# Performance work log

Measured on AMD Instinct MI355X. Metric: run time of the kernel, lower is better.

Reference implementation:

```python
import jax, jax.numpy as jnp
import numpy as np

WIN = 8     # sliding-chunk window size (Long2DSCSelfAttention default w=8)
HEADS = 8   # num_heads


def setup_inputs() -> dict:
    key = jax.random.key(0)
    ks = jax.random.split(key, 3)
    B, C, H, W = 4, 512, 64, 64
    x = jax.random.normal(ks[0], (B, C, H, W), jnp.float32)
    w_qkv = jax.random.normal(ks[1], (3 * C, C), jnp.float32) * 0.02
    b_qkv = jnp.zeros((3 * C,), jnp.float32)
    w_proj = jax.random.normal(ks[2], (C, C), jnp.float32) * 0.02
    b_proj = jnp.zeros((C,), jnp.float32)
    return {"x": x, "w_qkv": w_qkv, "b_qkv": b_qkv, "w_proj": w_proj, "b_proj": b_proj}


def _chunk(t, nh, nw, win):
    B, _, _, h, d = t.shape
    t = t.reshape(B, nh, win, nw, win, h, d)
    return t.transpose(0, 5, 1, 3, 2, 4, 6).reshape(B, h, nh, nw, win * win, d)


def reference(x, w_qkv, b_qkv, w_proj, b_proj):
    B, C, H, W = x.shape
    win, heads = WIN, HEADS
    d = C // heads
    nh, nw = H // win, W // win
    m = win * win  # tokens per chunk

    xf = x.transpose(0, 2, 3, 1)                      # [B,H,W,C]
    qkv = xf @ w_qkv.T + b_qkv                        # [B,H,W,3C]
    qkv = qkv.reshape(B, H, W, 3, heads, d)
    q = _chunk(qkv[..., 0, :, :], nh, nw, win)        # [B,h,nh,nw,m,d]
    k = _chunk(qkv[..., 1, :, :], nh, nw, win)
    v = _chunk(qkv[..., 2, :, :], nh, nw, win)

    # pad chunk grid by one chunk on each side; gather 3x3 chunk neighborhoods
    kp = jnp.pad(k, ((0, 0), (0, 0), (1, 1), (1, 1), (0, 0), (0, 0)))
    vp = jnp.pad(v, ((0, 0), (0, 0), (1, 1), (1, 1), (0, 0), (0, 0)))
    k9 = jnp.concatenate([kp[:, :, i:i + nh, j:j + nw] for i in range(3) for j in range(3)], axis=4)  # [B,h,nh,nw,9m,d]
    v9 = jnp.concatenate([vp[:, :, i:i + nh, j:j + nw] for i in range(3) for j in range(3)], axis=4)

    # validity mask for neighbor chunks at the image boundary
    valid = jnp.pad(jnp.ones((nh, nw), bool), ((1, 1), (1, 1)))
    vmask = jnp.concatenate(
        [jnp.repeat(valid[i:i + nh, j:j + nw][..., None], m, axis=-1) for i in range(3) for j in range(3)],
        axis=-1)                                      # [nh,nw,9m]

    scale = float(d) ** -0.5
    attn = jnp.einsum('bhxyqd,bhxykd->bhxyqk', q * scale, k9)      # [B,h,nh,nw,m,9m]
    neg = jnp.asarray(-1e9, attn.dtype)
    attn = jnp.where(vmask[None, None, :, :, None, :], attn, neg)
    attn = jax.nn.softmax(attn, axis=-1)
    out = jnp.einsum('bhxyqk,bhxykd->bhxyqd', attn, v9)            # [B,h,nh,nw,m,d]

    out = out.reshape(B, heads, nh, nw, win, win, d)
    out = out.transpose(0, 2, 4, 3, 5, 1, 6).reshape(B, H, W, C)
    out = out @ w_proj.T + b_proj
    return out.transpose(0, 3, 1, 2)                               # [B,C,H,W]
```

## Files before the change

kernel.cpp:

```cpp
#include <hip/hip_runtime.h>
#include <cstdint>
#include <cstddef>

namespace {

constexpr int kC = 512;
constexpr int kHW = 4096;
constexpr int kHeads = 8;
constexpr int kChunkElems = 64 * 64;

typedef float f32x4 __attribute__((ext_vector_type(4)));
typedef _Float16 f16x8 __attribute__((ext_vector_type(8)));
union FragU { uint4 u; f16x8 h; };

__device__ __forceinline__ ushort f16rn(float x) {
  _Float16 h = (_Float16)x;
  ushort u;
  __builtin_memcpy(&u, &h, 2);
  return u;
}
__device__ __forceinline__ uint pack2(ushort a, ushort b) {
  return (uint)a | ((uint)b << 16);
}
__device__ __forceinline__ float fexp2(float x) {
  return exp2f(x);
}
__device__ __forceinline__ uint pkrtz(float a, float b) {
  auto h = __builtin_amdgcn_cvt_pkrtz(a, b);
  uint u;
  __builtin_memcpy(&u, &h, 4);
  return u;
}
__device__ __forceinline__ void gld16(const void* g, void* lds) {
  __builtin_amdgcn_global_load_lds(
      (const __attribute__((address_space(1))) uint32_t*)g,
      (__attribute__((address_space(3))) uint32_t*)lds, 16, 0, 0);
}

__global__ __launch_bounds__(256)
void convw16_kernel(const float* __restrict__ w, ushort* __restrict__ wh)
{
  int idx = (blockIdx.x * 256 + threadIdx.x) * 8;
  float4 v0 = *(const float4*)(w + idx);
  float4 v1 = *(const float4*)(w + idx + 4);
  float xs[8] = {v0.x, v0.y, v0.z, v0.w, v1.x, v1.y, v1.z, v1.w};
  ushort hh[8];
#pragma unroll
  for (int e = 0; e < 8; ++e) hh[e] = f16rn(xs[e]);
  *(uint4*)(wh + idx) = make_uint4(pack2(hh[0], hh[1]), pack2(hh[2], hh[3]),
                                   pack2(hh[4], hh[5]), pack2(hh[6], hh[7]));
}

__global__ __launch_bounds__(256)
void convx_kernel(const float* __restrict__ x, ushort* __restrict__ xt)
{
  __shared__ float LT[64][68];
  const int tid = threadIdx.x;
  const int t0 = blockIdx.x * 64;
  const int c0 = blockIdx.y * 64;
  const int b  = blockIdx.z;
  const float* xb = x + (size_t)b * kC * kHW;

#pragma unroll
  for (int u = 0; u < 4; ++u) {
    int idx = tid + u * 256;
    int rc = idx >> 4;
    int t4 = (idx & 15) << 2;
    float4 val = *(const float4*)(xb + (size_t)(c0 + rc) * kHW + t0 + t4);
    LT[t4 + 0][rc] = val.x;
    LT[t4 + 1][rc] = val.y;
    LT[t4 + 2][rc] = val.z;
    LT[t4 + 3][rc] = val.w;
  }
  __syncthreads();
#pragma unroll
  for (int u = 0; u < 4; ++u) {
    int idx = tid + u * 256;
    int rt = idx >> 4;
    int c4 = (idx & 15) << 2;
    float4 v = *(const float4*)&LT[rt][c4];
    size_t o = ((size_t)b * kHW + t0 + rt) * kC + c0 + c4;
    *(ushort4*)(xt + o) = make_ushort4(f16rn(v.x), f16rn(v.y),
                                       f16rn(v.z), f16rn(v.w));
  }
}

__global__ __launch_bounds__(256)
void qkv_mfma_kernel(const ushort* __restrict__ xt,
                     const ushort* __restrict__ wq,
                     const float* __restrict__ bqkv,
                     ushort* __restrict__ qo, ushort* __restrict__ ko,
                     ushort* __restrict__ vo)
{
  __shared__ __align__(16) ushort As[2][128 * 64];
  __shared__ __align__(16) ushort Bs[2][128 * 64];

  const int tid  = threadIdx.x;
  const int lane = tid & 63;
  const int wv   = tid >> 6;
  const int quad = lane >> 4;
  const int l15  = lane & 15;
  const int wm = wv & 1, wn = wv >> 1;
  const int m0 = blockIdx.x * 128;
  const int n0 = blockIdx.y * 128;
  const int b  = blockIdx.z;

  const ushort* xb = xt + (size_t)b * kHW * kC;

  auto stage = [&](int buf, int k0) {
#pragma unroll
    for (int ii = 0; ii < 4; ++ii) {
      int i = wv * 4 + ii;
      int m = i * 8 + (lane >> 3);
      int gch = (lane & 7) ^ (m & 7);
      size_t goA = (size_t)(m0 + m) * kC + k0 + gch * 8;
      gld16(xb + goA, (char*)&As[buf][0] + i * 1024);
      size_t goB = (size_t)(n0 + m) * kC + k0 + gch * 8;
      gld16(wq + goB, (char*)&Bs[buf][0] + i * 1024);
    }
  };

  f32x4 acc[4][4];
#pragma unroll
  for (int i = 0; i < 4; ++i)
#pragma unroll
    for (int j = 0; j < 4; ++j) acc[i][j] = (f32x4){0.f, 0.f, 0.f, 0.f};

  stage(0, 0);
  asm volatile("s_waitcnt vmcnt(0)" ::: "memory");
  asm volatile("s_barrier" ::: "memory");

  for (int kt = 0; kt < 8; ++kt) {
    const int cur = kt & 1;
    if (kt < 7) stage(cur ^ 1, (kt + 1) * 64);

    const ushort* Ac = &As[cur][0];
    const ushort* Bc = &Bs[cur][0];
#pragma unroll
    for (int s = 0; s < 2; ++s) {
      const int gq = s * 4 + quad;
      FragU aA[4], bB[4];
#pragma unroll
      for (int mi = 0; mi < 4; ++mi) {
        int mr = wm * 64 + mi * 16 + l15;
        int off = mr * 64 + ((gq ^ (mr & 7)) * 8);
        aA[mi].u = *(const uint4*)&Ac[off];
      }
#pragma unroll
      for (int ni = 0; ni < 4; ++ni) {
        int nr = wn * 64 + ni * 16 + l15;
        int off = nr * 64 + ((gq ^ (nr & 7)) * 8);
        bB[ni].u = *(const uint4*)&Bc[off];
      }
#pragma unroll
      for (int mi = 0; mi < 4; ++mi)
#pragma unroll
        for (int ni = 0; ni < 4; ++ni)
          acc[mi][ni] = __builtin_amdgcn_mfma_f32_16x16x32_f16(aA[mi].h, bB[ni].h, acc[mi][ni], 0, 0, 0);
    }

    asm volatile("s_waitcnt lgkmcnt(0)" ::: "memory");
    if (kt < 7) asm volatile("s_waitcnt vmcnt(0)" ::: "memory");
    asm volatile("s_barrier" ::: "memory");
  }

  const int sec = n0 >> 9;
  const int jwbase = n0 + wn * 64;
  const int head = (jwbase >> 6) & 7;
  const size_t hbb = ((size_t)b * kHeads + head) * 64;
  float biasv[4];
#pragma unroll
  for (int ni = 0; ni < 4; ++ni) biasv[ni] = bqkv[jwbase + ni * 16 + l15];

  if (sec == 2) {
#pragma unroll
    for (int ni = 0; ni < 4; ++ni) {
      int dd = ni * 16 + l15;
#pragma unroll
      for (int mi = 0; mi < 4; ++mi) {
        int t0t = m0 + wm * 64 + mi * 16 + quad * 4;
        int h = t0t >> 6, w = t0t & 63;
        int cy = h >> 3, iy = h & 7, cx = w >> 3, ix = w & 7;
        size_t cb = (hbb + cy * 8 + cx) * (size_t)kChunkElems;
        int tokb = iy * 8 + ix;
        ushort hh[4];
#pragma unroll
        for (int r = 0; r < 4; ++r) hh[r] = f16rn(acc[mi][ni][r] + biasv[ni]);
        *(ushort4*)(vo + cb + (size_t)dd * 64 + tokb) = make_ushort4(hh[0], hh[1], hh[2], hh[3]);
      }
    }
  } else {
    ushort* dst = (sec == 0) ? qo : ko;
    const float sc = (sec == 0) ? 0.125f * 1.44269504089f : 1.0f;
    ushort* tH = &As[0][0] + wv * 1152;
    const int ltok = lane >> 2;
    const int dd0 = (lane & 3) * 16;
#pragma unroll
    for (int mi = 0; mi < 4; ++mi) {
#pragma unroll
      for (int ni = 0; ni < 4; ++ni)
#pragma unroll
        for (int r = 0; r < 4; ++r)
          tH[(quad * 4 + r) * 68 + ni * 16 + l15] =
              f16rn((acc[mi][ni][r] + biasv[ni]) * sc);
      int tg = m0 + wm * 64 + mi * 16 + ltok;
      int h = tg >> 6, w = tg & 63;
      int cy = h >> 3, iy = h & 7, cx = w >> 3, ix = w & 7;
      size_t cb = (hbb + cy * 8 + cx) * (size_t)kChunkElems
                + (size_t)(iy * 8 + ix) * 64 + dd0;
      uint4 h0 = *(const uint4*)&tH[ltok * 68 + dd0];
      uint4 h1 = *(const uint4*)&tH[ltok * 68 + dd0 + 8];
      *(uint4*)(dst + cb) = h0;
      *(uint4*)(dst + cb + 8) = h1;
    }
  }
}

__global__ __launch_bounds__(256)
void attn_mfma_kernel(const ushort* __restrict__ qg, const ushort* __restrict__ kg,
                      const ushort* __restrict__ vg,
                      ushort* __restrict__ ao)
{
  __shared__ __align__(16) ushort KB[4096], VB[4096];
  __shared__ __align__(16) ushort Ps[4 * 16 * 72];

  const int tid  = threadIdx.x;
  const int lane = tid & 63;
  const int wv   = tid >> 6;
  const int quad = lane >> 4;
  const int l15  = lane & 15;

  const int bx = blockIdx.x;
  const int g  = (bx & 7) * 4 + ((bx >> 3) >> 6);
  const int c  = (bx >> 3) & 63;
  const int b = g >> 3, head = g & 7;
  const int cy = c >> 3, cx = c & 7;

  const size_t hb = (size_t)b * kHeads + head;
  const size_t gbase = hb * 64 * (size_t)kChunkElems;
  const size_t cbase = gbase + (size_t)c * (size_t)kChunkElems;

  FragU aQ0, aQ1;
  {
    const ushort* qr = qg + cbase + (size_t)(wv * 16 + l15) * 64 + quad * 8;
    aQ0.u = *(const uint4*)(qr);
    aQ1.u = *(const uint4*)(qr + 32);
  }

  const int boff = ((lane >> 3) * 64) + (((lane & 7) ^ (lane >> 3)) * 8);
  const ushort* kgB = kg + gbase + boff + (size_t)(wv * 2) * 512;
  const ushort* vgB = vg + gbase + boff + (size_t)(wv * 2) * 512;
  char* kDst0 = (char*)KB + (wv * 2) * 1024;
  char* vDst0 = (char*)VB + (wv * 2) * 1024;

  int kvOff0[4], kvOff1[4];
  {
    const int sw = l15 & 7;
#pragma unroll
    for (int nt = 0; nt < 4; ++nt) {
      int row = nt * 16 + l15;
      kvOff0[nt] = row * 64 + ((quad ^ sw) * 8);
      kvOff1[nt] = row * 64 + (((4 + quad) ^ sw) * 8);
    }
  }

  ushort* PsW = Ps + wv * 1152;
  ushort* pWr = PsW + l15 * 72 + quad * 4;
  const ushort* pRd = PsW + l15 * 72 + quad * 8;

  unsigned long long list = 0ull;
  int cnt = 0;
#pragma unroll
  for (int p = 0; p < 9; ++p) {
    const int dy = p / 3 - 1, dx = p % 3 - 1;
    int ny = cy + dy, nx = cx + dx;
    if ((unsigned)ny < 8u && (unsigned)nx < 8u) {
      list |= (unsigned long long)(ny * 8 + nx) << (6 * cnt);
      ++cnt;
    }
  }

  f32x4 o[4];
#pragma unroll
  for (int r = 0; r < 4; ++r) o[r] = (f32x4){0.f, 0.f, 0.f, 0.f};
  float rsum = 0.f;

  {
    int ch0 = (int)(list & 63);
    const ushort* pk = kgB + (size_t)ch0 * kChunkElems;
    gld16(pk, kDst0);
    gld16(pk + 512, kDst0 + 1024);
    const ushort* pv = vgB + (size_t)ch0 * kChunkElems;
    gld16(pv, vDst0);
    gld16(pv + 512, vDst0 + 1024);
  }

  for (int i = 0; i < cnt; ++i) {
    const bool more = (i + 1 < cnt);
    const int chn = (int)((list >> (6 * (i + 1))) & 63);

    asm volatile("s_waitcnt vmcnt(2)" ::: "memory");
    asm volatile("s_barrier" ::: "memory");

    FragU kf[8];
#pragma unroll
    for (int nt = 0; nt < 4; ++nt) {
      kf[nt * 2].u     = *(const uint4*)&KB[kvOff0[nt]];
      kf[nt * 2 + 1].u = *(const uint4*)&KB[kvOff1[nt]];
    }
    asm volatile("s_waitcnt lgkmcnt(0)" ::: "memory");
    asm volatile("s_waitcnt vmcnt(0)" ::: "memory");
    asm volatile("s_barrier" ::: "memory");

    if (more) {
      const ushort* pk = kgB + (size_t)chn * kChunkElems;
      gld16(pk, kDst0);
      gld16(pk + 512, kDst0 + 1024);
    }

    f32x4 s[4];
#pragma unroll
    for (int nt = 0; nt < 4; ++nt) s[nt] = (f32x4){0.f, 0.f, 0.f, 0.f};
#pragma unroll
    for (int nt = 0; nt < 4; ++nt) {
      s[nt] = __builtin_amdgcn_mfma_f32_16x16x32_f16(kf[nt * 2].h, aQ0.h, s[nt], 0, 0, 0);
      s[nt] = __builtin_amdgcn_mfma_f32_16x16x32_f16(kf[nt * 2 + 1].h, aQ1.h, s[nt], 0, 0, 0);
    }

#pragma unroll
    for (int nt = 0; nt < 4; ++nt) {
      float e0 = fexp2(s[nt][0]);
      float e1 = fexp2(s[nt][1]);
      float e2 = fexp2(s[nt][2]);
      float e3 = fexp2(s[nt][3]);
      rsum += (e0 + e1) + (e2 + e3);
      *(uint2*)(pWr + nt * 16) = make_uint2(pkrtz(e0, e1), pkrtz(e2, e3));
    }

    FragU aP0, aP1;
    aP0.u = *(const uint4*)(pRd);
    aP1.u = *(const uint4*)(pRd + 32);

#pragma unroll
    for (int nt = 0; nt < 4; ++nt) {
      FragU v0, v1;
      v0.u = *(const uint4*)&VB[kvOff0[nt]];
      v1.u = *(const uint4*)&VB[kvOff1[nt]];
      o[nt] = __builtin_amdgcn_mfma_f32_16x16x32_f16(v0.h, aP0.h, o[nt], 0, 0, 0);
      o[nt] = __builtin_amdgcn_mfma_f32_16x16x32_f16(v1.h, aP1.h, o[nt], 0, 0, 0);
    }

    asm volatile("s_waitcnt lgkmcnt(0)" ::: "memory");
    asm volatile("s_barrier" ::: "memory");
    if (more) {
      const ushort* pv = vgB + (size_t)chn * kChunkElems;
      gld16(pv, vDst0);
      gld16(pv + 512, vDst0 + 1024);
    }
  }

  rsum += __shfl_xor(rsum, 16, 64);
  rsum += __shfl_xor(rsum, 32, 64);
  const float inv = 1.0f / rsum;

  const int trg = wv * 16 + l15;
  const int hp = cy * 8 + (trg >> 3);
  const int wp = cx * 8 + (trg & 7);
  const size_t obase = ((size_t)b * kHW + hp * 64 + wp) * (size_t)kC + head * 64;

#pragma unroll
  for (int nt = 0; nt < 4; ++nt) {
    float v0 = o[nt][0] * inv;
    float v1 = o[nt][1] * inv;
    float v2 = o[nt][2] * inv;
    float v3 = o[nt][3] * inv;
    *(ushort4*)(ao + obase + nt * 16 + quad * 4) =
        make_ushort4(f16rn(v0), f16rn(v1), f16rn(v2), f16rn(v3));
  }
}

__global__ __launch_bounds__(256)
void proj_mfma_kernel(const ushort* __restrict__ ao,
                      const ushort* __restrict__ wp,
                      const float* __restrict__ bproj,
                      float* __restrict__ out)
{
  __shared__ __align__(16) ushort As[2][128 * 64];
  __shared__ __align__(16) ushort Bs[2][64 * 64];

  const int tid  = threadIdx.x;
  const int lane = tid & 63;
  const int wv   = tid >> 6;
  const int quad = lane >> 4;
  const int l15  = lane & 15;
  const int wm = wv & 1, wn = wv >> 1;
  const int n0g = blockIdx.x * 64;
  const int m0  = blockIdx.y * 128;
  const int b   = n0g >> 12;
  const int tl0 = n0g & 4095;

  auto stage = [&](int buf, int k0) {
#pragma unroll
    for (int ii = 0; ii < 4; ++ii) {
      int i = wv * 4 + ii;
      int m = i * 8 + (lane >> 3);
      int gch = (lane & 7) ^ (m & 7);
      size_t goA = (size_t)(m0 + m) * kC + k0 + gch * 8;
      gld16(wp + goA, (char*)&As[buf][0] + i * 1024);
    }
#pragma unroll
    for (int ii = 0; ii < 2; ++ii) {
      int i = wv * 2 + ii;
      int m = i * 8 + (lane >> 3);
      int gch = (lane & 7) ^ (m & 7);
      size_t goB = (size_t)(n0g + m) * kC + k0 + gch * 8;
      gld16(ao + goB, (char*)&Bs[buf][0] + i * 1024);
    }
  };

  f32x4 acc[4][2];
#pragma unroll
  for (int i = 0; i < 4; ++i)
#pragma unroll
    for (int j = 0; j < 2; ++j) acc[i][j] = (f32x4){0.f, 0.f, 0.f, 0.f};

  stage(0, 0);
  asm volatile("s_waitcnt vmcnt(0)" ::: "memory");
  asm volatile("s_barrier" ::: "memory");

  for (int kt = 0; kt < 8; ++kt) {
    const int cur = kt & 1;
    if (kt < 7) stage(cur ^ 1, (kt + 1) * 64);

    const ushort* Ac = &As[cur][0];
    const ushort* Bc = &Bs[cur][0];
#pragma unroll
    for (int s = 0; s < 2; ++s) {
      const int gq = s * 4 + quad;
      FragU aA[4], bB[2];
#pragma unroll
      for (int mi = 0; mi < 4; ++mi) {
        int mr = wm * 64 + mi * 16 + l15;
        int off = mr * 64 + ((gq ^ (mr & 7)) * 8);
        aA[mi].u = *(const uint4*)&Ac[off];
      }
#pragma unroll
      for (int ni = 0; ni < 2; ++ni) {
        int nr = wn * 32 + ni * 16 + l15;
        int off = nr * 64 + ((gq ^ (nr & 7)) * 8);
        bB[ni].u = *(const uint4*)&Bc[off];
      }
#pragma unroll
      for (int mi = 0; mi < 4; ++mi)
#pragma unroll
        for (int ni = 0; ni < 2; ++ni)
          acc[mi][ni] = __builtin_amdgcn_mfma_f32_16x16x32_f16(aA[mi].h, bB[ni].h, acc[mi][ni], 0, 0, 0);
    }

    asm volatile("s_waitcnt lgkmcnt(0)" ::: "memory");
    if (kt < 7) asm volatile("s_waitcnt vmcnt(0)" ::: "memory");
    asm volatile("s_barrier" ::: "memory");
  }

#pragma unroll
  for (int mi = 0; mi < 4; ++mi)
#pragma unroll
    for (int r = 0; r < 4; ++r) {
      int c = m0 + wm * 64 + mi * 16 + quad * 4 + r;
      float bias = bproj[c];
      size_t rowb = ((size_t)b * kC + c) * (size_t)kHW + tl0 + wn * 32;
#pragma unroll
      for (int ni = 0; ni < 2; ++ni)
        out[rowb + ni * 16 + l15] = acc[mi][ni][r] + bias;
    }
}

}

extern "C" void kernel_launch(void* const* d_in, const int* in_sizes, int n_in,
                              void* d_out, int out_size, void* d_ws, size_t ws_size,
                              hipStream_t stream)
{
  const float* x     = (const float*)d_in[0];
  const float* wqkv  = (const float*)d_in[1];
  const float* bqkv  = (const float*)d_in[2];
  const float* wproj = (const float*)d_in[3];
  const float* bproj = (const float*)d_in[4];
  float* out = (float*)d_out;

  const size_t seg = (size_t)2048 * kChunkElems;
  ushort* base = (ushort*)d_ws;
  ushort* qb = base + 0 * seg;
  ushort* kb = base + 1 * seg;
  ushort* vb = base + 2 * seg;
  ushort* xt = base + 3 * seg;
  ushort* ao = xt;
  ushort* wqh = base + 5 * seg;
  ushort* wp16 = qb;

  convw16_kernel<<<dim3(384), 256, 0, stream>>>(wqkv, wqh);
  convx_kernel<<<dim3(64, 8, 4), 256, 0, stream>>>(x, xt);
  qkv_mfma_kernel<<<dim3(32, 12, 4), 256, 0, stream>>>(xt, wqh, bqkv,
                                                       qb, kb, vb);
  attn_mfma_kernel<<<dim3(2048), 256, 0, stream>>>(qb, kb, vb, ao);
  convw16_kernel<<<dim3(128), 256, 0, stream>>>(wproj, wp16);
  proj_mfma_kernel<<<dim3(256, 4), 256, 0, stream>>>(ao, wp16, bproj, out);
}
```

Before: 192.3 us.

## Enlarge QKV GEMM tile to 256x128 with 512 threads and swizzled block order

The QKV projection GEMM now runs 512-thread blocks computing 256x128 output tiles, so each staged weight tile is reused across twice as many rows. A flattened block-index swizzle reorders tiles to improve L2 locality. All LDS fragments for both k-substeps are loaded up front, and the MFMA section runs under raised wave priority. The larger tile raises LDS use and per-block register pressure, which may lower occupancy. The epilogue must still map the 4x2 wave layout correctly.

```diff
diff --git a/kernel.cpp b/kernel.cpp
--- a/kernel.cpp
+++ b/kernel.cpp
@@ -85,14 +85,14 @@
   }
 }
 
-__global__ __launch_bounds__(256)
+__global__ __launch_bounds__(512)
 void qkv_mfma_kernel(const ushort* __restrict__ xt,
                      const ushort* __restrict__ wq,
                      const float* __restrict__ bqkv,
                      ushort* __restrict__ qo, ushort* __restrict__ ko,
                      ushort* __restrict__ vo)
 {
-  __shared__ __align__(16) ushort As[2][128 * 64];
+  __shared__ __align__(16) ushort As[2][256 * 64];
   __shared__ __align__(16) ushort Bs[2][128 * 64];
 
   const int tid  = threadIdx.x;
@@ -100,10 +100,15 @@
   const int wv   = tid >> 6;
   const int quad = lane >> 4;
   const int l15  = lane & 15;
-  const int wm = wv & 1, wn = wv >> 1;
-  const int m0 = blockIdx.x * 128;
-  const int n0 = blockIdx.y * 128;
-  const int b  = blockIdx.z;
+  const int wm = wv & 3;
+  const int wn = wv >> 2;
+
+  const int flat = blockIdx.x + 16 * (blockIdx.y + 12 * blockIdx.z);
+  const int swz  = (flat & 7) * 96 + (flat >> 3);
+  const int m0 = (swz & 15) * 256;
+  const int t2 = swz >> 4;
+  const int n0 = (t2 % 12) * 128;
+  const int b  = t2 / 12;
 
   const ushort* xb = xt + (size_t)b * kHW * kC;
 
@@ -113,10 +118,16 @@
       int i = wv * 4 + ii;
       int m = i * 8 + (lane >> 3);
       int gch = (lane & 7) ^ (m & 7);
-      size_t goA = (size_t)(m0 + m) * kC + k0 + gch * 8;
-      gld16(xb + goA, (char*)&As[buf][0] + i * 1024);
-      size_t goB = (size_t)(n0 + m) * kC + k0 + gch * 8;
-      gld16(wq + goB, (char*)&Bs[buf][0] + i * 1024);
+      gld16(xb + (size_t)(m0 + m) * kC + k0 + gch * 8,
+            (char*)&As[buf][0] + i * 1024);
+    }
+#pragma unroll
+    for (int ii = 0; ii < 2; ++ii) {
+      int i = wv * 2 + ii;
+      int m = i * 8 + (lane >> 3);
+      int gch = (lane & 7) ^ (m & 7);
+      gld16(wq + (size_t)(n0 + m) * kC + k0 + gch * 8,
+            (char*)&Bs[buf][0] + i * 1024);
     }
   };
 
@@ -136,28 +147,33 @@
 
     const ushort* Ac = &As[cur][0];
     const ushort* Bc = &Bs[cur][0];
-#pragma unroll
-    for (int s = 0; s < 2; ++s) {
-      const int gq = s * 4 + quad;
-      FragU aA[4], bB[4];
-#pragma unroll
-      for (int mi = 0; mi < 4; ++mi) {
-        int mr = wm * 64 + mi * 16 + l15;
-        int off = mr * 64 + ((gq ^ (mr & 7)) * 8);
-        aA[mi].u = *(const uint4*)&Ac[off];
-      }
-#pragma unroll
-      for (int ni = 0; ni < 4; ++ni) {
-        int nr = wn * 64 + ni * 16 + l15;
-        int off = nr * 64 + ((gq ^ (nr & 7)) * 8);
-        bB[ni].u = *(const uint4*)&Bc[off];
-      }
-#pragma unroll
-      for (int mi = 0; mi < 4; ++mi)
-#pragma unroll
-        for (int ni = 0; ni < 4; ++ni)
-          acc[mi][ni] = __builtin_amdgcn_mfma_f32_16x16x32_f16(aA[mi].h, bB[ni].h, acc[mi][ni], 0, 0, 0);
-    }
+    FragU a0[4], a1[4], b0[4], b1[4];
+#pragma unroll
+    for (int mi = 0; mi < 4; ++mi) {
+      int mr = wm * 64 + mi * 16 + l15;
+      int sw = mr & 7;
+      a0[mi].u = *(const uint4*)&Ac[mr * 64 + ((quad ^ sw) * 8)];
+      a1[mi].u = *(const uint4*)&Ac[mr * 64 + (((4 + quad) ^ sw) * 8)];
+    }
+#pragma unroll
+    for (int ni = 0; ni < 4; ++ni) {
+      int nr = wn * 64 + ni * 16 + l15;
+      int sw = nr & 7;
+      b0[ni].u = *(const uint4*)&Bc[nr * 64 + ((quad ^ sw) * 8)];
+      b1[ni].u = *(const uint4*)&Bc[nr * 64 + (((4 + quad) ^ sw) * 8)];
+    }
+    __builtin_amdgcn_s_setprio(1);
+#pragma unroll
+    for (int mi = 0; mi < 4; ++mi)
+#pragma unroll
+      for (int ni = 0; ni < 4; ++ni)
+        acc[mi][ni] = __builtin_amdgcn_mfma_f32_16x16x32_f16(a0[mi].h, b0[ni].h, acc[mi][ni], 0, 0, 0);
+#pragma unroll
+    for (int mi = 0; mi < 4; ++mi)
+#pragma unroll
+      for (int ni = 0; ni < 4; ++ni)
+        acc[mi][ni] = __builtin_amdgcn_mfma_f32_16x16x32_f16(a1[mi].h, b1[ni].h, acc[mi][ni], 0, 0, 0);
+    __builtin_amdgcn_s_setprio(0);
 
     asm volatile("s_waitcnt lgkmcnt(0)" ::: "memory");
     if (kt < 7) asm volatile("s_waitcnt vmcnt(0)" ::: "memory");
@@ -500,7 +516,7 @@
 
   convw16_kernel<<<dim3(384), 256, 0, stream>>>(wqkv, wqh);
   convx_kernel<<<dim3(64, 8, 4), 256, 0, stream>>>(x, xt);
-  qkv_mfma_kernel<<<dim3(32, 12, 4), 256, 0, stream>>>(xt, wqh, bqkv,
+  qkv_mfma_kernel<<<dim3(16, 12, 4), 512, 0, stream>>>(xt, wqh, bqkv,
                                                        qb, kb, vb);
   attn_mfma_kernel<<<dim3(2048), 256, 0, stream>>>(qb, kb, vb, ao);
   convw16_kernel<<<dim3(128), 256, 0, stream>>>(wproj, wp16);
```

Result: slower. 196.2 us (+2.1%).
